# Kernel tuning notes

Hardware: AMD Instinct MI355X
Metric: run time of the kernel (lower is better)

Reference implementation:

```python
import jax, jax.numpy as jnp
import numpy as np

N = 50000
E = 800000
H = 128

def setup_inputs() -> dict:
    key = jax.random.key(0)
    ks = jax.random.split(key, 12)
    s = 1.0 / np.sqrt(H)
    inp = {
        "x": jax.random.normal(ks[0], (N, H), dtype=jnp.float32),
        "edge_index": jax.random.randint(ks[1], (2, E), 0, N, dtype=jnp.int64),
        "edge_attr": jax.random.normal(ks[2], (E, H), dtype=jnp.float32),
        # linear_edge: Linear(3H, H)
        "We": jax.random.uniform(ks[3], (3 * H, H), jnp.float32, -s, s),
        "be": jnp.zeros((H,), jnp.float32),
        # attention_layer.W: Linear(H, H)
        "Wg": jax.random.uniform(ks[4], (H, H), jnp.float32, -s, s),
        "bg": jnp.zeros((H,), jnp.float32),
        # attention_layer.a: Linear(2H, 1)
        "Wa": jax.random.uniform(ks[5], (2 * H, 1), jnp.float32, -s, s),
        "ba": jnp.zeros((1,), jnp.float32),
        # linear_out: Linear(H, H)
        "Wo": jax.random.uniform(ks[6], (H, H), jnp.float32, -s, s),
        "bo": jnp.zeros((H,), jnp.float32),
    }
    return inp


def reference(x, edge_index, edge_attr, We, be, Wg, bg, Wa, ba, Wo, bo):
    # PyG MessagePassing (flow=source_to_target): j = edge_index[0] (source),
    # i = edge_index[1] (target); aggregation scatters to edge_index[1].
    src = edge_index[0]
    dst = edge_index[1]

    # message: SiLU(Linear(cat[x_i, x_j, edge_attr]))  -- split We to avoid a [E,3H] concat
    m = jax.nn.silu(x[dst] @ We[:H] + x[src] @ We[H:2 * H] + edge_attr @ We[2 * H:] + be)  # [E,H]
    agg = jax.ops.segment_sum(m, dst, num_segments=N)  # [N,H] scatter-add aggregate

    # GraphAttentionLayer: row, col = edge_index -> row=edge_index[0], col=edge_index[1]
    h = agg @ Wg + bg  # [N,H]
    score = jax.nn.leaky_relu(h[src] @ Wa[:H] + h[dst] @ Wa[H:] + ba, negative_slope=0.2)  # [E,1]
    # softmax over the last dim of size 1 -> all ones (faithful to original); dropout off (eval)
    alpha = jax.nn.softmax(score, axis=-1)  # [E,1]
    attn_out = jax.ops.segment_sum(alpha * h[dst], src, num_segments=N)  # [N,H]

    return attn_out @ Wo + bo  # linear_out
```

## Files before the change

### kernel.cpp

```cpp
#include <hip/hip_runtime.h>

#define N_NODES 50000
#define N_EDGES 800000
#define HDIM 128

typedef unsigned short u16;
typedef unsigned int u32;
typedef __attribute__((ext_vector_type(8))) short short8;
typedef __attribute__((ext_vector_type(4))) float f32x4;
typedef __attribute__((ext_vector_type(2))) float f32x2;

__device__ __forceinline__ u16 f2bf(float f) {
    union { float f; u32 u; } v; v.f = f;
    u32 r = v.u + 0x7FFFu + ((v.u >> 16) & 1u);
    return (u16)(r >> 16);
}

__device__ __forceinline__ float bf2f(u16 h) {
    union { u32 u; float f; } v; v.u = ((u32)h) << 16;
    return v.f;
}

__global__ __launch_bounds__(256) void pack_b(const float* __restrict__ src,
                                              u16* __restrict__ dst, int tOff) {
    int f = threadIdx.x + blockIdx.x * 256;
    if (f >= 2048) return;
    int t = f >> 8;
    int c = (f >> 6) & 3;
    int lane = f & 63;
    int q = lane >> 4, n = lane & 15;
    const float* s = src + (size_t)(c * 32 + q * 8) * 128 + t * 16 + n;
    u16* dp = dst + ((((size_t)(t + tOff) * 4 + c) * 64 + lane) * 8);
#pragma unroll
    for (int j = 0; j < 8; ++j) dp[j] = f2bf(s[(size_t)j * 128]);
}

__global__ void build_bias256(const float* __restrict__ be, float* __restrict__ b256) {
    int i = threadIdx.x;
    b256[i] = (i < 128) ? be[i] : 0.f;
}

__global__ __launch_bounds__(256) void hist_kernel(const int* __restrict__ srcIdx,
                                                   const int* __restrict__ dstIdx,
                                                   int* __restrict__ degD,
                                                   int* __restrict__ degS) {
    int e = blockIdx.x * 256 + threadIdx.x;
    if (e >= N_EDGES) return;
    atomicAdd(&degD[dstIdx[e]], 1);
    atomicAdd(&degS[srcIdx[e]], 1);
}

__global__ __launch_bounds__(256) void scan_kernel(const int* __restrict__ deg,
                                                   int* __restrict__ off,
                                                   int* __restrict__ cur) {
    __shared__ int buf[256];
    const int CHUNK = 196;
    int tid = threadIdx.x;
    int s0 = tid * CHUNK, s1 = s0 + CHUNK;
    if (s1 > N_NODES) s1 = N_NODES;
    int s = 0;
    for (int i = s0; i < s1; ++i) s += deg[i];
    buf[tid] = s;
    __syncthreads();
    for (int o = 1; o < 256; o <<= 1) {
        int v = (tid >= o) ? buf[tid - o] : 0;
        __syncthreads();
        buf[tid] += v;
        __syncthreads();
    }
    int run = (tid > 0) ? buf[tid - 1] : 0;
    for (int i = s0; i < s1; ++i) {
        off[i] = run;
        cur[i] = run;
        run += deg[i];
    }
    if (tid == 255) off[N_NODES] = buf[255];
}

__global__ __launch_bounds__(256) void scatter_kernel(const int* __restrict__ srcIdx,
                                                      const int* __restrict__ dstIdx,
                                                      int* __restrict__ curD,
                                                      int* __restrict__ curS,
                                                      int* __restrict__ sd_ea,
                                                      int* __restrict__ sd_src,
                                                      int* __restrict__ ss_dst) {
    int e = blockIdx.x * 256 + threadIdx.x;
    if (e >= N_EDGES) return;
    int s = srcIdx[e], d = dstIdx[e];
    int p = atomicAdd(&curD[d], 1);
    sd_ea[p] = e;
    sd_src[p] = s;
    int p2 = atomicAdd(&curS[s], 1);
    ss_dst[p2] = d;
}

__global__ __launch_bounds__(256) void gemm_mfma(const void* __restrict__ Ap,
                                                 const u16* __restrict__ PB,
                                                 const float* __restrict__ bias,
                                                 void* __restrict__ outp,
                                                 int M, int Ctiles, int flags) {
    int tid = threadIdx.x;
    int wave = tid >> 6;
    int lane = tid & 63;
    int strip = blockIdx.x * 4 + wave;
    int row0 = strip * 16;
    if (row0 >= M) return;
    int q = lane >> 4, n = lane & 15;
    int C = Ctiles * 16;

    short8 a[4];
    if (flags & 2) {
        const u16* ap = (const u16*)Ap + (size_t)(row0 + n) * 128 + q * 8;
#pragma unroll
        for (int c = 0; c < 4; ++c) a[c] = *(const short8*)(ap + c * 32);
    } else {
        const float* ap = (const float*)Ap + (size_t)(row0 + n) * 128 + q * 8;
#pragma unroll
        for (int c = 0; c < 4; ++c) {
            f32x4 f0 = *(const f32x4*)(ap + c * 32);
            f32x4 f1 = *(const f32x4*)(ap + c * 32 + 4);
            short8 t;
#pragma unroll
            for (int j = 0; j < 4; ++j) {
                t[j] = (short)f2bf(f0[j]);
                t[4 + j] = (short)f2bf(f1[j]);
            }
            a[c] = t;
        }
    }

    for (int t = 0; t < Ctiles; ++t) {
        f32x4 acc = {0.f, 0.f, 0.f, 0.f};
#pragma unroll
        for (int c = 0; c < 4; ++c) {
            short8 b = *(const short8*)(PB + (((size_t)t * 4 + c) * 64 + lane) * 8);
            acc = __builtin_amdgcn_mfma_f32_16x16x32_bf16(a[c], b, acc, 0, 0, 0);
        }
        int col = t * 16 + n;
        float bv = bias ? bias[col] : 0.f;
#pragma unroll
        for (int r = 0; r < 4; ++r) {
            int row = row0 + q * 4 + r;
            float v = acc[r] + bv;
            if (flags & 1)
                ((u16*)outp)[(size_t)row * C + col] = f2bf(v);
            else
                ((float*)outp)[(size_t)row * C + col] = v;
        }
    }
}

__global__ __launch_bounds__(256) void agg_fused(const float* __restrict__ EA,
                                                 const u16* __restrict__ PB3,
                                                 const int* __restrict__ offD,
                                                 const int* __restrict__ sd_ea,
                                                 const int* __restrict__ sd_src,
                                                 const u16* __restrict__ T1,
                                                 u16* __restrict__ agg) {
    int tid = threadIdx.x;
    int wave = tid >> 6;
    int lane = tid & 63;
    int node = blockIdx.x * 4 + wave;
    if (node >= N_NODES) return;
    int q = lane >> 4, n = lane & 15;
    int segS = offD[node], segE = offD[node + 1];

    float g1[8], rowAcc[8];
#pragma unroll
    for (int t = 0; t < 8; ++t) {
        g1[t] = bf2f(T1[(size_t)node * 256 + t * 16 + n]);
        rowAcc[t] = 0.f;
    }

    for (int base = segS; base < segE; base += 16) {
        int er = base + n;
        if (er > segE - 1) er = segE - 1;
        const float* ap = EA + (size_t)sd_ea[er] * 128 + q * 8;
        short8 a[4];
#pragma unroll
        for (int c = 0; c < 4; ++c) {
            f32x4 f0 = *(const f32x4*)(ap + c * 32);
            f32x4 f1 = *(const f32x4*)(ap + c * 32 + 4);
            short8 t;
#pragma unroll
            for (int j = 0; j < 4; ++j) {
                t[j] = (short)f2bf(f0[j]);
                t[4 + j] = (short)f2bf(f1[j]);
            }
            a[c] = t;
        }
        int srow[4];
        bool val[4];
#pragma unroll
        for (int r = 0; r < 4; ++r) {
            int idx = base + q * 4 + r;
            val[r] = idx < segE;
            srow[r] = val[r] ? sd_src[idx] : 0;
        }
#pragma unroll
        for (int t = 0; t < 8; ++t) {
            f32x4 acc = {0.f, 0.f, 0.f, 0.f};
#pragma unroll
            for (int c = 0; c < 4; ++c) {
                short8 b = *(const short8*)(PB3 + (((size_t)t * 4 + c) * 64 + lane) * 8);
                acc = __builtin_amdgcn_mfma_f32_16x16x32_bf16(a[c], b, acc, 0, 0, 0);
            }
            int col = t * 16 + n;
#pragma unroll
            for (int r = 0; r < 4; ++r) {
                float v = acc[r] + g1[t] + bf2f(T1[(size_t)srow[r] * 256 + 128 + col]);
                float m = v / (1.f + __expf(-v));
                rowAcc[t] += val[r] ? m : 0.f;
            }
        }
    }
#pragma unroll
    for (int t = 0; t < 8; ++t) {
        float v = rowAcc[t];
        v += __shfl_xor(v, 16, 64);
        v += __shfl_xor(v, 32, 64);
        if (lane < 16) agg[(size_t)node * 128 + t * 16 + lane] = f2bf(v);
    }
}

__global__ __launch_bounds__(256) void attn_gather(const int* __restrict__ offS,
                                                   const int* __restrict__ ss_dst,
                                                   const u16* __restrict__ h,
                                                   float* __restrict__ attn) {
    int tid = threadIdx.x;
    int wave = tid >> 6;
    int lane = tid & 63;
    int node = blockIdx.x * 4 + wave;
    if (node >= N_NODES) return;
    int e0 = offS[node], e1 = offS[node + 1];
    float a0 = 0.f, a1 = 0.f;
    int d_next = (e0 < e1) ? ss_dst[e0] : 0;
    for (int e = e0; e < e1;) {
        int d = d_next;
        ++e;
        d_next = (e < e1) ? ss_dst[e] : 0;
        u32 hv = *(const u32*)(h + (size_t)d * 128 + lane * 2);
        a0 += bf2f((u16)(hv & 0xFFFFu));
        a1 += bf2f((u16)(hv >> 16));
    }
    f32x2 o;
    o[0] = a0;
    o[1] = a1;
    *(f32x2*)(attn + (size_t)node * 128 + lane * 2) = o;
}

extern "C" void kernel_launch(void* const* d_in, const int* in_sizes, int n_in,
                              void* d_out, int out_size, void* d_ws, size_t ws_size,
                              hipStream_t stream) {
    const float* x  = (const float*)d_in[0];
    const int* ei   = (const int*)d_in[1];
    const float* ea = (const float*)d_in[2];
    const float* We = (const float*)d_in[3];
    const float* be = (const float*)d_in[4];
    const float* Wg = (const float*)d_in[5];
    const float* bg = (const float*)d_in[6];
    const float* Wo = (const float*)d_in[9];
    const float* bo = (const float*)d_in[10];
    float* out = (float*)d_out;

    const int* srcIdx = ei;
    const int* dstIdx = ei + N_EDGES;

    char* ws = (char*)d_ws;
    u16*   PB1    = (u16*)(ws + 0);
    u16*   PB3    = (u16*)(ws + 65536);
    u16*   PBg    = (u16*)(ws + 98304);
    u16*   PBo    = (u16*)(ws + 131072);
    float* bias256 = (float*)(ws + 163840);
    u16*   T1     = (u16*)(ws + 262144);
    float* attn   = (float*)(ws + 262144);
    u16*   agg    = (u16*)(ws + 25862144);
    u16*   hbuf   = (u16*)(ws + 38662144);
    int*   degD   = (int*)(ws + 51462144);
    int*   degS   = (int*)(ws + 51662144);
    int*   offD   = (int*)(ws + 51862144);
    int*   offS   = (int*)(ws + 52062160);
    int*   curD   = (int*)(ws + 52262176);
    int*   curS   = (int*)(ws + 52462176);
    int*   sd_ea  = (int*)(ws + 52662176);
    int*   sd_src = (int*)(ws + 55862176);
    int*   ss_dst = (int*)(ws + 59062176);

    hipMemsetAsync(degD, 0, 400000, stream);

    pack_b<<<8, 256, 0, stream>>>(We, PB1, 0);
    pack_b<<<8, 256, 0, stream>>>(We + 128 * 128, PB1, 8);
    pack_b<<<8, 256, 0, stream>>>(We + 2 * 128 * 128, PB3, 0);
    pack_b<<<8, 256, 0, stream>>>(Wg, PBg, 0);
    pack_b<<<8, 256, 0, stream>>>(Wo, PBo, 0);
    build_bias256<<<1, 256, 0, stream>>>(be, bias256);

    hist_kernel<<<3125, 256, 0, stream>>>(srcIdx, dstIdx, degD, degS);
    scan_kernel<<<1, 256, 0, stream>>>(degD, offD, curD);
    scan_kernel<<<1, 256, 0, stream>>>(degS, offS, curS);
    scatter_kernel<<<3125, 256, 0, stream>>>(srcIdx, dstIdx, curD, curS, sd_ea, sd_src, ss_dst);

    gemm_mfma<<<782, 256, 0, stream>>>(x, PB1, bias256, T1, N_NODES, 16, 1);

    agg_fused<<<12500, 256, 0, stream>>>(ea, PB3, offD, sd_ea, sd_src, T1, agg);

    gemm_mfma<<<782, 256, 0, stream>>>(agg, PBg, bg, hbuf, N_NODES, 8, 3);

    attn_gather<<<12500, 256, 0, stream>>>(offS, ss_dst, hbuf, attn);

    gemm_mfma<<<782, 256, 0, stream>>>(attn, PBo, bo, out, N_NODES, 8, 0);

    (void)in_sizes; (void)n_in; (void)out_size; (void)ws_size;
}
```

Baseline: 1.290 ms.

## Fold Wo into Wg, drop final GEMM, interleave T1 layout, merge setup kernels

Precomputes Wg·Wo and bg·Wo so the output projection runs before the source-side gather, which removes the final GEMM and the fp32 attn buffer. The gather now adds bo and writes the output directly, with its edge loop unrolled by four. T1 is stored column-interleaved so agg_fused can load each gathered neighbour row with one vector load. Edge id and source id are packed into an int2, and the source ids are broadcast by shuffle instead of re-read. Setup kernels are also merged: the three We packs become one launch and the two scans become one two-block launch. The intermediate h2 is now bf16 after the combined projection, which changes rounding behaviour.

```diff
diff --git a/kernel.cpp b/kernel.cpp
--- a/kernel.cpp
+++ b/kernel.cpp
@@ -21,13 +21,10 @@
     return v.f;
 }
 
-__global__ __launch_bounds__(256) void pack_b(const float* __restrict__ src,
-                                              u16* __restrict__ dst, int tOff) {
-    int f = threadIdx.x + blockIdx.x * 256;
-    if (f >= 2048) return;
-    int t = f >> 8;
-    int c = (f >> 6) & 3;
-    int lane = f & 63;
+__device__ __forceinline__ void pack_one(const float* src, u16* dst, int g, int tOff) {
+    int t = g >> 8;
+    int c = (g >> 6) & 3;
+    int lane = g & 63;
     int q = lane >> 4, n = lane & 15;
     const float* s = src + (size_t)(c * 32 + q * 8) * 128 + t * 16 + n;
     u16* dp = dst + ((((size_t)(t + tOff) * 4 + c) * 64 + lane) * 8);
@@ -35,9 +32,46 @@
     for (int j = 0; j < 8; ++j) dp[j] = f2bf(s[(size_t)j * 128]);
 }
 
+__global__ __launch_bounds__(256) void pack_we(const float* __restrict__ We,
+                                               u16* __restrict__ PB1,
+                                               u16* __restrict__ PB3) {
+    int f = blockIdx.x * 256 + threadIdx.x;
+    int m = f >> 11;
+    int g = f & 2047;
+    if (m == 0)      pack_one(We,               PB1, g, 0);
+    else if (m == 1) pack_one(We + 16384,       PB1, g, 8);
+    else             pack_one(We + 32768,       PB3, g, 0);
+}
+
+__global__ __launch_bounds__(256) void pack_b(const float* __restrict__ src,
+                                              u16* __restrict__ dst) {
+    int g = blockIdx.x * 256 + threadIdx.x;
+    if (g < 2048) pack_one(src, dst, g, 0);
+}
+
 __global__ void build_bias256(const float* __restrict__ be, float* __restrict__ b256) {
     int i = threadIdx.x;
     b256[i] = (i < 128) ? be[i] : 0.f;
+}
+
+__global__ __launch_bounds__(256) void compute_wgo(const float* __restrict__ Wg,
+                                                   const float* __restrict__ Wo,
+                                                   const float* __restrict__ bg,
+                                                   float* __restrict__ Wgo,
+                                                   float* __restrict__ bgo) {
+    int id = blockIdx.x * 256 + threadIdx.x;
+    if (id < 16384) {
+        int i = id >> 7, j = id & 127;
+        float s = 0.f;
+#pragma unroll 8
+        for (int k = 0; k < 128; ++k) s += Wg[i * 128 + k] * Wo[k * 128 + j];
+        Wgo[id] = s;
+    }
+    if (id < 128) {
+        float s = 0.f;
+        for (int k = 0; k < 128; ++k) s += bg[k] * Wo[k * 128 + id];
+        bgo[id] = s;
+    }
 }
 
 __global__ __launch_bounds__(256) void hist_kernel(const int* __restrict__ srcIdx,
@@ -50,19 +84,24 @@
     atomicAdd(&degS[srcIdx[e]], 1);
 }
 
-__global__ __launch_bounds__(256) void scan_kernel(const int* __restrict__ deg,
-                                                   int* __restrict__ off,
-                                                   int* __restrict__ cur) {
-    __shared__ int buf[256];
-    const int CHUNK = 196;
+__global__ __launch_bounds__(1024) void scan_both(const int* __restrict__ degD,
+                                                  const int* __restrict__ degS,
+                                                  int* __restrict__ offD, int* __restrict__ offS,
+                                                  int* __restrict__ curD, int* __restrict__ curS) {
+    __shared__ int buf[1024];
+    const int CHUNK = 49;
+    const int* deg = blockIdx.x ? degS : degD;
+    int* off = blockIdx.x ? offS : offD;
+    int* cur = blockIdx.x ? curS : curD;
     int tid = threadIdx.x;
     int s0 = tid * CHUNK, s1 = s0 + CHUNK;
+    if (s0 > N_NODES) s0 = N_NODES;
     if (s1 > N_NODES) s1 = N_NODES;
     int s = 0;
     for (int i = s0; i < s1; ++i) s += deg[i];
     buf[tid] = s;
     __syncthreads();
-    for (int o = 1; o < 256; o <<= 1) {
+    for (int o = 1; o < 1024; o <<= 1) {
         int v = (tid >= o) ? buf[tid - o] : 0;
         __syncthreads();
         buf[tid] += v;
@@ -74,22 +113,22 @@
         cur[i] = run;
         run += deg[i];
     }
-    if (tid == 255) off[N_NODES] = buf[255];
-}
+    if (tid == 1023) off[N_NODES] = buf[1023];
+}
+
+typedef struct { int e, s; } EdgePair;
 
 __global__ __launch_bounds__(256) void scatter_kernel(const int* __restrict__ srcIdx,
                                                       const int* __restrict__ dstIdx,
                                                       int* __restrict__ curD,
                                                       int* __restrict__ curS,
-                                                      int* __restrict__ sd_ea,
-                                                      int* __restrict__ sd_src,
+                                                      int2* __restrict__ sd,
                                                       int* __restrict__ ss_dst) {
     int e = blockIdx.x * 256 + threadIdx.x;
     if (e >= N_EDGES) return;
     int s = srcIdx[e], d = dstIdx[e];
     int p = atomicAdd(&curD[d], 1);
-    sd_ea[p] = e;
-    sd_src[p] = s;
+    sd[p] = make_int2(e, s);
     int p2 = atomicAdd(&curS[s], 1);
     ss_dst[p2] = d;
 }
@@ -138,25 +177,26 @@
         }
         int col = t * 16 + n;
         float bv = bias ? bias[col] : 0.f;
+        int ocol = col;
+        if (flags & 4) ocol = (col & ~127) + (col & 15) * 8 + ((col & 127) >> 4);
 #pragma unroll
         for (int r = 0; r < 4; ++r) {
             int row = row0 + q * 4 + r;
             float v = acc[r] + bv;
             if (flags & 1)
-                ((u16*)outp)[(size_t)row * C + col] = f2bf(v);
+                ((u16*)outp)[(size_t)row * C + ocol] = f2bf(v);
             else
-                ((float*)outp)[(size_t)row * C + col] = v;
-        }
-    }
-}
-
-__global__ __launch_bounds__(256) void agg_fused(const float* __restrict__ EA,
-                                                 const u16* __restrict__ PB3,
-                                                 const int* __restrict__ offD,
-                                                 const int* __restrict__ sd_ea,
-                                                 const int* __restrict__ sd_src,
-                                                 const u16* __restrict__ T1,
-                                                 u16* __restrict__ agg) {
+                ((float*)outp)[(size_t)row * C + ocol] = v;
+        }
+    }
+}
+
+__global__ __launch_bounds__(256, 4) void agg_fused(const float* __restrict__ EA,
+                                                    const u16* __restrict__ PB3,
+                                                    const int* __restrict__ offD,
+                                                    const int2* __restrict__ sd,
+                                                    const u16* __restrict__ T1,
+                                                    u16* __restrict__ agg) {
     int tid = threadIdx.x;
     int wave = tid >> 6;
     int lane = tid & 63;
@@ -165,17 +205,20 @@
     int q = lane >> 4, n = lane & 15;
     int segS = offD[node], segE = offD[node + 1];
 
+    short8 g1v = *(const short8*)(T1 + (size_t)node * 256 + n * 8);
     float g1[8], rowAcc[8];
 #pragma unroll
     for (int t = 0; t < 8; ++t) {
-        g1[t] = bf2f(T1[(size_t)node * 256 + t * 16 + n]);
+        g1[t] = bf2f((u16)g1v[t]);
         rowAcc[t] = 0.f;
     }
 
     for (int base = segS; base < segE; base += 16) {
         int er = base + n;
         if (er > segE - 1) er = segE - 1;
-        const float* ap = EA + (size_t)sd_ea[er] * 128 + q * 8;
+        int2 es = sd[er];
+
+        const float* ap = EA + (size_t)es.x * 128 + q * 8;
         short8 a[4];
 #pragma unroll
         for (int c = 0; c < 4; ++c) {
@@ -189,14 +232,20 @@
             }
             a[c] = t;
         }
+
         int srow[4];
         bool val[4];
+        short8 tb[4];
 #pragma unroll
         for (int r = 0; r < 4; ++r) {
             int idx = base + q * 4 + r;
             val[r] = idx < segE;
-            srow[r] = val[r] ? sd_src[idx] : 0;
-        }
+            srow[r] = __shfl(es.y, q * 4 + r, 16);
+        }
+#pragma unroll
+        for (int r = 0; r < 4; ++r)
+            tb[r] = *(const short8*)(T1 + (size_t)srow[r] * 256 + 128 + n * 8);
+
 #pragma unroll
         for (int t = 0; t < 8; ++t) {
             f32x4 acc = {0.f, 0.f, 0.f, 0.f};
@@ -205,10 +254,9 @@
                 short8 b = *(const short8*)(PB3 + (((size_t)t * 4 + c) * 64 + lane) * 8);
                 acc = __builtin_amdgcn_mfma_f32_16x16x32_bf16(a[c], b, acc, 0, 0, 0);
             }
-            int col = t * 16 + n;
 #pragma unroll
             for (int r = 0; r < 4; ++r) {
-                float v = acc[r] + g1[t] + bf2f(T1[(size_t)srow[r] * 256 + 128 + col]);
+                float v = acc[r] + g1[t] + bf2f((u16)tb[r][t]);
                 float m = v / (1.f + __expf(-v));
                 rowAcc[t] += val[r] ? m : 0.f;
             }
@@ -219,14 +267,20 @@
         float v = rowAcc[t];
         v += __shfl_xor(v, 16, 64);
         v += __shfl_xor(v, 32, 64);
-        if (lane < 16) agg[(size_t)node * 128 + t * 16 + lane] = f2bf(v);
-    }
-}
-
-__global__ __launch_bounds__(256) void attn_gather(const int* __restrict__ offS,
-                                                   const int* __restrict__ ss_dst,
-                                                   const u16* __restrict__ h,
-                                                   float* __restrict__ attn) {
+        rowAcc[t] = v;
+    }
+#pragma unroll
+    for (int u = 0; u < 2; ++u) {
+        int t = q * 2 + u;
+        agg[(size_t)node * 128 + t * 16 + n] = f2bf(rowAcc[t]);
+    }
+}
+
+__global__ __launch_bounds__(256) void out_gather(const int* __restrict__ offS,
+                                                  const int* __restrict__ ss_dst,
+                                                  const u16* __restrict__ h2,
+                                                  const float* __restrict__ bo,
+                                                  float* __restrict__ out) {
     int tid = threadIdx.x;
     int wave = tid >> 6;
     int lane = tid & 63;
@@ -234,19 +288,28 @@
     if (node >= N_NODES) return;
     int e0 = offS[node], e1 = offS[node + 1];
     float a0 = 0.f, a1 = 0.f;
-    int d_next = (e0 < e1) ? ss_dst[e0] : 0;
-    for (int e = e0; e < e1;) {
-        int d = d_next;
-        ++e;
-        d_next = (e < e1) ? ss_dst[e] : 0;
-        u32 hv = *(const u32*)(h + (size_t)d * 128 + lane * 2);
-        a0 += bf2f((u16)(hv & 0xFFFFu));
+    int e = e0;
+    for (; e + 4 <= e1; e += 4) {
+        int d0 = ss_dst[e], d1 = ss_dst[e + 1], d2 = ss_dst[e + 2], d3 = ss_dst[e + 3];
+        u32 h0 = *(const u32*)(h2 + (size_t)d0 * 128 + lane * 2);
+        u32 h1 = *(const u32*)(h2 + (size_t)d1 * 128 + lane * 2);
+        u32 hh2 = *(const u32*)(h2 + (size_t)d2 * 128 + lane * 2);
+        u32 h3 = *(const u32*)(h2 + (size_t)d3 * 128 + lane * 2);
+        a0 += bf2f((u16)h0) + bf2f((u16)h1) + bf2f((u16)hh2) + bf2f((u16)h3);
+        a1 += bf2f((u16)(h0 >> 16)) + bf2f((u16)(h1 >> 16)) +
+              bf2f((u16)(hh2 >> 16)) + bf2f((u16)(h3 >> 16));
+    }
+    for (; e < e1; ++e) {
+        int d = ss_dst[e];
+        u32 hv = *(const u32*)(h2 + (size_t)d * 128 + lane * 2);
+        a0 += bf2f((u16)hv);
         a1 += bf2f((u16)(hv >> 16));
     }
+    f32x2 bv = *(const f32x2*)(bo + lane * 2);
     f32x2 o;
-    o[0] = a0;
-    o[1] = a1;
-    *(f32x2*)(attn + (size_t)node * 128 + lane * 2) = o;
+    o[0] = a0 + bv[0];
+    o[1] = a1 + bv[1];
+    *(f32x2*)(out + (size_t)node * 128 + lane * 2) = o;
 }
 
 extern "C" void kernel_launch(void* const* d_in, const int* in_sizes, int n_in,
@@ -267,48 +330,42 @@
     const int* dstIdx = ei + N_EDGES;
 
     char* ws = (char*)d_ws;
-    u16*   PB1    = (u16*)(ws + 0);
-    u16*   PB3    = (u16*)(ws + 65536);
-    u16*   PBg    = (u16*)(ws + 98304);
-    u16*   PBo    = (u16*)(ws + 131072);
-    float* bias256 = (float*)(ws + 163840);
-    u16*   T1     = (u16*)(ws + 262144);
-    float* attn   = (float*)(ws + 262144);
-    u16*   agg    = (u16*)(ws + 25862144);
-    u16*   hbuf   = (u16*)(ws + 38662144);
-    int*   degD   = (int*)(ws + 51462144);
-    int*   degS   = (int*)(ws + 51662144);
-    int*   offD   = (int*)(ws + 51862144);
-    int*   offS   = (int*)(ws + 52062160);
-    int*   curD   = (int*)(ws + 52262176);
-    int*   curS   = (int*)(ws + 52462176);
-    int*   sd_ea  = (int*)(ws + 52662176);
-    int*   sd_src = (int*)(ws + 55862176);
-    int*   ss_dst = (int*)(ws + 59062176);
+    u16*   PB1     = (u16*)(ws + 0);
+    u16*   PB3     = (u16*)(ws + 65536);
+    u16*   PBgo    = (u16*)(ws + 98304);
+    float* bias256 = (float*)(ws + 131072);
+    float* Wgo     = (float*)(ws + 132096);
+    float* bgo     = (float*)(ws + 197632);
+    u16*   T1      = (u16*)(ws + 262144);
+    u16*   agg     = (u16*)(ws + 25862144);
+    u16*   h2      = (u16*)(ws + 38662144);
+    int*   degD    = (int*)(ws + 51462144);
+    int*   degS    = (int*)(ws + 51662144);
+    int*   offD    = (int*)(ws + 51862144);
+    int*   offS    = (int*)(ws + 52062160);
+    int*   curD    = (int*)(ws + 52262176);
+    int*   curS    = (int*)(ws + 52462176);
+    int2*  sd      = (int2*)(ws + 52662176);
+    int*   ss_dst  = (int*)(ws + 59062176);
 
     hipMemsetAsync(degD, 0, 400000, stream);
 
-    pack_b<<<8, 256, 0, stream>>>(We, PB1, 0);
-    pack_b<<<8, 256, 0, stream>>>(We + 128 * 128, PB1, 8);
-    pack_b<<<8, 256, 0, stream>>>(We + 2 * 128 * 128, PB3, 0);
-    pack_b<<<8, 256, 0, stream>>>(Wg, PBg, 0);
-    pack_b<<<8, 256, 0, stream>>>(Wo, PBo, 0);
+    pack_we<<<24, 256, 0, stream>>>(We, PB1, PB3);
     build_bias256<<<1, 256, 0, stream>>>(be, bias256);
+    compute_wgo<<<64, 256, 0, stream>>>(Wg, Wo, bg, Wgo, bgo);
+    pack_b<<<8, 256, 0, stream>>>(Wgo, PBgo);
 
     hist_kernel<<<3125, 256, 0, stream>>>(srcIdx, dstIdx, degD, degS);
-    scan_kernel<<<1, 256, 0, stream>>>(degD, offD, curD);
-    scan_kernel<<<1, 256, 0, stream>>>(degS, offS, curS);
-    scatter_kernel<<<3125, 256, 0, stream>>>(srcIdx, dstIdx, curD, curS, sd_ea, sd_src, ss_dst);
-
-    gemm_mfma<<<782, 256, 0, stream>>>(x, PB1, bias256, T1, N_NODES, 16, 1);
-
-    agg_fused<<<12500, 256, 0, stream>>>(ea, PB3, offD, sd_ea, sd_src, T1, agg);
-
-    gemm_mfma<<<782, 256, 0, stream>>>(agg, PBg, bg, hbuf, N_NODES, 8, 3);
-
-    attn_gather<<<12500, 256, 0, stream>>>(offS, ss_dst, hbuf, attn);
-
-    gemm_mfma<<<782, 256, 0, stream>>>(attn, PBo, bo, out, N_NODES, 8, 0);
+    scan_both<<<2, 1024, 0, stream>>>(degD, degS, offD, offS, curD, curS);
+    scatter_kernel<<<3125, 256, 0, stream>>>(srcIdx, dstIdx, curD, curS, sd, ss_dst);
+
+    gemm_mfma<<<782, 256, 0, stream>>>(x, PB1, bias256, T1, N_NODES, 16, 1 | 4);
+
+    agg_fused<<<12500, 256, 0, stream>>>(ea, PB3, offD, sd, T1, agg);
+
+    gemm_mfma<<<782, 256, 0, stream>>>(agg, PBgo, bgo, h2, N_NODES, 8, 1 | 2);
+
+    out_gather<<<12500, 256, 0, stream>>>(offS, ss_dst, h2, bo, out);
 
     (void)in_sizes; (void)n_in; (void)out_size; (void)ws_size;
 }
```

After: 1.447 ms. 1.12x slower.
